# Optimization experiments

Measured on AMD Instinct MI355X. Metric: run time of the kernel, lower is better.

Reference implementation:

```python
import jax, jax.numpy as jnp
import numpy as np

EPS = 1e-8


def setup_inputs() -> dict:
    key = jax.random.key(0)
    ks = jax.random.split(key, 9)
    b, f, n1, n2 = 32, 256, 64, 256
    inp = {
        "search_feats": jax.random.normal(ks[0], (b, f, n2), jnp.float32),
        "template_feats": jax.random.normal(ks[1], (b, f, n1), jnp.float32),
        "template_seeds": jax.random.normal(ks[2], (b, n1, 3), jnp.float32),
        # SharedMLP (1x1 conv2d) weights: channels 260 -> 256 -> 256 -> 256
        "W1": jax.random.normal(ks[3], (256, 260), jnp.float32) * 0.05,
        "b1": jnp.zeros((256,), jnp.float32),
        "W2": jax.random.normal(ks[4], (256, 256), jnp.float32) * 0.05,
        "b2": jnp.zeros((256,), jnp.float32),
        "W3": jax.random.normal(ks[5], (256, 256), jnp.float32) * 0.05,
        "b3": jnp.zeros((256,), jnp.float32),
        # conv1d chain (kernel size 1): 256 -> 256 (ReLU) -> 256 (no act)
        "W4": jax.random.normal(ks[6], (256, 256), jnp.float32) * 0.05,
        "b4": jnp.zeros((256,), jnp.float32),
        "W5": jax.random.normal(ks[7], (256, 256), jnp.float32) * 0.05,
        "b5": jnp.zeros((256,), jnp.float32),
    }
    return inp


def reference(search_feats, template_feats, template_seeds,
              W1, b1, W2, b2, W3, b3, W4, b4, W5, b5):
    b, f, n2 = search_feats.shape
    n1 = template_feats.shape[-1]

    # Cosine similarity along feature dim (torch clamps each norm to eps).
    t_norm = template_feats / jnp.maximum(
        jnp.linalg.norm(template_feats, axis=1, keepdims=True), EPS)
    s_norm = search_feats / jnp.maximum(
        jnp.linalg.norm(search_feats, axis=1, keepdims=True), EPS)
    sim = jnp.einsum('bfn,bfm->bnm', t_norm, s_norm)  # (b, n1, n2)

    # Build fusion feature (b, 1+3+f, n1, n2) via broadcasting (no copies needed).
    xyz = jnp.transpose(template_seeds, (0, 2, 1))  # (b, 3, n1)
    xyz_b = jnp.broadcast_to(xyz[:, :, :, None], (b, 3, n1, n2))
    tf_b = jnp.broadcast_to(template_feats[:, :, :, None], (b, f, n1, n2))
    fusion = jnp.concatenate([sim[:, None], xyz_b, tf_b], axis=1)  # (b, 260, n1, n2)

    # SharedMLP: 1x1 conv2d + ReLU per layer
    x = jax.nn.relu(jnp.einsum('oc,bcnm->bonm', W1, fusion) + b1[None, :, None, None])
    x = jax.nn.relu(jnp.einsum('oc,bcnm->bonm', W2, x) + b2[None, :, None, None])
    x = jax.nn.relu(jnp.einsum('oc,bcnm->bonm', W3, x) + b3[None, :, None, None])

    # max_pool2d over n1 dim (kernel [n1, 1]) then squeeze -> (b, 256, n2)
    x = jnp.max(x, axis=2)

    # conv1d chain (kernel size 1)
    x = jax.nn.relu(jnp.einsum('oc,bcm->bom', W4, x) + b4[None, :, None])
    x = jnp.einsum('oc,bcm->bom', W5, x) + b5[None, :, None]
    return x
```

## Files before the change

kernel.cpp:

```cpp
#include <hip/hip_runtime.h>
#include <math.h>

#define BB 32
#define FF 256
#define N1 64
#define N2 256

typedef _Float16 f16;
typedef _Float16 f16x4 __attribute__((ext_vector_type(4)));
typedef _Float16 f16x8 __attribute__((ext_vector_type(8)));
typedef float f32x4 __attribute__((ext_vector_type(4)));

#define OFFB_W14T 0u
#define OFFB_W1H  45056u
#define OFFB_W2H  176128u
#define OFFB_W3H  307200u
#define OFFB_W4H  438272u
#define OFFB_W5H  569344u

__global__ void k_prep(const float* __restrict__ W1, const float* __restrict__ W2,
                       const float* __restrict__ W3, const float* __restrict__ W4,
                       const float* __restrict__ W5, char* __restrict__ wsb) {
  int x = blockIdx.x, m = blockIdx.y, t = threadIdx.x;
  int idx = x * 256 + t;
  if (m == 0)      ((f16*)(wsb + OFFB_W2H))[idx] = (f16)W2[idx];
  else if (m == 1) ((f16*)(wsb + OFFB_W3H))[idx] = (f16)W3[idx];
  else if (m == 2) ((f16*)(wsb + OFFB_W4H))[idx] = (f16)W4[idx];
  else if (m == 3) ((f16*)(wsb + OFFB_W5H))[idx] = (f16)W5[idx];
  else if (m == 4) ((f16*)(wsb + OFFB_W1H))[idx] = (f16)W1[x * 260 + 4 + t];
  else if (x < 4)  ((float*)(wsb + OFFB_W14T))[x * 256 + t] = W1[t * 260 + x];
}


#define LD(S, KS, MF) (*(const f16x8*)((S) + ((KS) * 2 + (MF)) * 1024 + lane * 16))

#define ZERO_ACC                                                  \
  _Pragma("unroll") for (int of = 0; of < 4; ++of)                \
  _Pragma("unroll") for (int mf = 0; mf < 2; ++mf)                \
      acc[of][mf] = (f32x4){0.f, 0.f, 0.f, 0.f};

#define GEMM4(SRC)                                                                \
  {                                                                               \
    f16x8 a0 = LD(SRC, 0, 0), a1 = LD(SRC, 0, 1);                                 \
    f16x8 p0 = LD(SRC, 1, 0), p1 = LD(SRC, 1, 1);                                 \
    __builtin_amdgcn_s_setprio(1);                                                \
    _Pragma("unroll") for (int ks = 0; ks < 8; ++ks) {                            \
      f16x8 c0 = a0, c1 = a1;                                                     \
      a0 = p0; a1 = p1;                                                           \
      if (ks < 6) { p0 = LD(SRC, ks + 2, 0); p1 = LD(SRC, ks + 2, 1); }           \
      _Pragma("unroll") for (int of = 0; of < 4; ++of) {                          \
        acc[of][0] = __builtin_amdgcn_mfma_f32_16x16x32_f16(wreg[of][ks], c0,     \
                                                            acc[of][0], 0, 0, 0); \
        acc[of][1] = __builtin_amdgcn_mfma_f32_16x16x32_f16(wreg[of][ks], c1,     \
                                                            acc[of][1], 0, 0, 0); \
      }                                                                           \
    }                                                                             \
    __builtin_amdgcn_s_setprio(0);                                                \
  }

#define STORE_FRAG(DST)                                                           \
  _Pragma("unroll") for (int of = 0; of < 4; ++of)                                \
  _Pragma("unroll") for (int mf = 0; mf < 2; ++mf) {                              \
    f16x4 hv;                                                                     \
    _Pragma("unroll") for (int j = 0; j < 4; ++j)                                 \
        hv[j] = (f16)fmaxf(acc[of][mf][j] + biasv[of][j], 0.f);                   \
    *(f16x4*)((DST) + ((wg * 2 + (of >> 1)) * 2 + mf) * 1024 +                    \
              ((of & 1) * 2 + (g >> 1)) * 256 + r * 16 + (g & 1) * 8) = hv;       \
  }

#define POOLUP                                                                    \
  _Pragma("unroll") for (int of = 0; of < 4; ++of)                                \
  _Pragma("unroll") for (int mf = 0; mf < 2; ++mf)                                \
  _Pragma("unroll") for (int j = 0; j < 4; ++j) {                                 \
    f16 hv = (f16)fmaxf(acc[of][mf][j] + biasv[of][j], 0.f);                      \
    if (hv > pool[of][mf][j]) pool[of][mf][j] = hv;                               \
  }

#define PRODUCE_Y1(NN, DST)                                                       \
  {                                                                               \
    float sv0 = sml[(NN) * 32 + r];                                               \
    float sv1 = sml[(NN) * 32 + 16 + r];                                          \
    f16x8 c8 = *(const f16x8*)(c1h + (NN) * 264 + w * 32 + g * 8);                \
    f16x8 h0, h1;                                                                 \
    _Pragma("unroll") for (int q = 0; q < 4; ++q) {                               \
      float ca = (float)c8[q], cb = (float)c8[4 + q];                             \
      h0[q] = (f16)fmaxf(fmaf(w1a[q], sv0, ca), 0.f);                             \
      h0[4 + q] = (f16)fmaxf(fmaf(w1b[q], sv0, cb), 0.f);                         \
      h1[q] = (f16)fmaxf(fmaf(w1a[q], sv1, ca), 0.f);                             \
      h1[4 + q] = (f16)fmaxf(fmaf(w1b[q], sv1, cb), 0.f);                         \
    }                                                                             \
    *(f16x8*)((DST) + (w * 2) * 1024 + lane * 16) = h0;                           \
    *(f16x8*)((DST) + (w * 2 + 1) * 1024 + lane * 16) = h1;                       \
  }

__global__ __launch_bounds__(512, 2) void k_mega(
    const float* __restrict__ sf, const float* __restrict__ tf,
    const float* __restrict__ seeds, const float* __restrict__ b1,
    const float* __restrict__ b2, const float* __restrict__ b3,
    const float* __restrict__ b4, const float* __restrict__ b5,
    const char* __restrict__ wsb, float* __restrict__ out) {
  const int mt = blockIdx.x, b = blockIdx.y, mb = mt * 32;
  const int tid = threadIdx.x;
  const int w = tid >> 6, lane = tid & 63, g = lane >> 4, r = lane & 15;
  const int grp = w >> 2, wg = w & 3;

  const float* w14t = (const float*)(wsb + OFFB_W14T);
  const f16* w1h = (const f16*)(wsb + OFFB_W1H);
  const f16* w2h = (const f16*)(wsb + OFFB_W2H);
  const f16* w3h = (const f16*)(wsb + OFFB_W3H);
  const f16* w4h = (const f16*)(wsb + OFFB_W4H);
  const f16* w5h = (const f16*)(wsb + OFFB_W5H);

  __shared__ __align__(16) char yl[65536];
  __shared__ __align__(16) f16 c1h[64 * 264];
  __shared__ __align__(16) float sml[64 * 32];
  __shared__ __align__(16) float part_t[64 * 8];
  __shared__ __align__(16) float part_s[32 * 16];
  __shared__ float invt_l[64];
  __shared__ float invs_l[32];
#define Y1BUF(i) (yl + (i) * 16384)
#define Y2BUF(i) (yl + 32768 + (i) * 16384)

  float tv[32];
  {
    const int n = lane;
    float ssq = 0.f;
#pragma unroll
    for (int j = 0; j < 4; ++j) {
      int oct = j * 8 + w;
#pragma unroll
      for (int e = 0; e < 8; ++e) {
        float v = tf[((size_t)b * FF + oct * 8 + e) * N1 + n];
        tv[j * 8 + e] = v;
        ssq = fmaf(v, v, ssq);
      }
    }
    part_t[n * 8 + w] = ssq;
  }
  float sv2[16];
  {
    const int m = tid & 31, q = tid >> 5;
    float ssq = 0.f;
#pragma unroll
    for (int j = 0; j < 2; ++j) {
      int oct = j * 16 + q;
#pragma unroll
      for (int e = 0; e < 8; ++e) {
        float v = sf[((size_t)b * FF + oct * 8 + e) * N2 + mb + m];
        sv2[j * 8 + e] = v;
        ssq = fmaf(v, v, ssq);
      }
    }
    part_s[m * 16 + q] = ssq;
  }
  __syncthreads();
  if (tid < 64) {
    float a = 0.f;
#pragma unroll
    for (int i = 0; i < 8; ++i) a += part_t[tid * 8 + i];
    invt_l[tid] = 1.0f / fmaxf(sqrtf(a), 1e-8f);
  }
  if (tid < 32) {
    float a = 0.f;
#pragma unroll
    for (int i = 0; i < 16; ++i) a += part_s[tid * 16 + i];
    invs_l[tid] = 1.0f / fmaxf(sqrtf(a), 1e-8f);
  }
  __syncthreads();
  {
    const int n = lane;
#pragma unroll
    for (int j = 0; j < 4; ++j) {
      int oct = j * 8 + w;
      f16x8 h;
#pragma unroll
      for (int e = 0; e < 8; ++e) h[e] = (f16)tv[j * 8 + e];
      *(f16x8*)(yl + ((oct >> 2) * 4 + (n >> 4)) * 1024 +
                ((oct & 3) * 16 + (n & 15)) * 16) = h;
    }
  }
  {
    const int m = tid & 31, q = tid >> 5;
    float iv = invs_l[m];
#pragma unroll
    for (int j = 0; j < 2; ++j) {
      int oct = j * 16 + q;
      f16x8 h;
#pragma unroll
      for (int e = 0; e < 8; ++e) h[e] = (f16)(sv2[j * 8 + e] * iv);
      *(f16x8*)(yl + 32768 + ((oct >> 2) * 2 + (m >> 4)) * 1024 +
                ((oct & 3) * 16 + (m & 15)) * 16) = h;
    }
  }
  __syncthreads();

  {
    const int nt = w >> 1, mfs = w & 1;
    f32x4 sa = {0.f, 0.f, 0.f, 0.f};
#pragma unroll
    for (int ks = 0; ks < 8; ++ks) {
      f16x8 af = *(const f16x8*)(yl + (ks * 4 + nt) * 1024 + lane * 16);
      f16x8 bfm = *(const f16x8*)(yl + 32768 + (ks * 2 + mfs) * 1024 + lane * 16);
      sa = __builtin_amdgcn_mfma_f32_16x16x32_f16(af, bfm, sa, 0, 0, 0);
    }
#pragma unroll
    for (int j = 0; j < 4; ++j) {
      int n = nt * 16 + g * 4 + j;
      sml[n * 32 + mfs * 16 + r] = sa[j] * invt_l[n];
    }
  }
  {
    f16x8 w1f[2][8];
#pragma unroll
    for (int ofl = 0; ofl < 2; ++ofl)
#pragma unroll
      for (int ks = 0; ks < 8; ++ks)
        w1f[ofl][ks] = *(const f16x8*)(w1h + (w * 32 + ofl * 16 + r) * 256 +
                                       ks * 32 + g * 8);
    f32x4 ac[2][4];
#pragma unroll
    for (int ofl = 0; ofl < 2; ++ofl)
#pragma unroll
      for (int nf = 0; nf < 4; ++nf) ac[ofl][nf] = (f32x4){0.f, 0.f, 0.f, 0.f};
#pragma unroll
    for (int ks = 0; ks < 8; ++ks)
#pragma unroll
      for (int nf = 0; nf < 4; ++nf) {
        f16x8 bfm = *(const f16x8*)(yl + (ks * 4 + nf) * 1024 + lane * 16);
        ac[0][nf] = __builtin_amdgcn_mfma_f32_16x16x32_f16(w1f[0][ks], bfm,
                                                           ac[0][nf], 0, 0, 0);
        ac[1][nf] = __builtin_amdgcn_mfma_f32_16x16x32_f16(w1f[1][ks], bfm,
                                                           ac[1][nf], 0, 0, 0);
      }
    f32x4 b1v[2], wx[2], wy[2], wz[2];
#pragma unroll
    for (int ofl = 0; ofl < 2; ++ofl) {
      int o = w * 32 + ofl * 16 + g * 4;
      b1v[ofl] = *(const f32x4*)(b1 + o);
      wx[ofl] = *(const f32x4*)(w14t + 256 + o);
      wy[ofl] = *(const f32x4*)(w14t + 512 + o);
      wz[ofl] = *(const f32x4*)(w14t + 768 + o);
    }
#pragma unroll
    for (int nf = 0; nf < 4; ++nf) {
      int n = nf * 16 + r;
      const float* sd = seeds + ((size_t)b * 64 + n) * 3;
      float sx = sd[0], sy = sd[1], sz = sd[2];
#pragma unroll
      for (int ofl = 0; ofl < 2; ++ofl) {
        f16x4 hv;
#pragma unroll
        for (int j = 0; j < 4; ++j)
          hv[j] = (f16)(ac[ofl][nf][j] + b1v[ofl][j] + wx[ofl][j] * sx +
                        wy[ofl][j] * sy + wz[ofl][j] * sz);
        *(f16x4*)(c1h + n * 264 + w * 32 + ofl * 16 + g * 4) = hv;
      }
    }
  }
  __syncthreads();

  f16x8 wreg[4][8];
  f32x4 biasv[4];
  f16x4 pool[4][2];
  f32x4 acc[4][2];
  f32x4 w1a, w1b;
  {
    const f16* wsrc = grp ? w3h : w2h;
    const float* bsrc = grp ? b3 : b2;
#pragma unroll
    for (int of = 0; of < 4; ++of) {
#pragma unroll
      for (int ks = 0; ks < 8; ++ks)
        wreg[of][ks] = *(const f16x8*)(wsrc + (wg * 64 + of * 16 + r) * 256 +
                                       ks * 32 + g * 8);
      biasv[of] = *(const f32x4*)(bsrc + wg * 64 + of * 16 + g * 4);
    }
    w1a = *(const f32x4*)(w14t + w * 32 + g * 8);
    w1b = *(const f32x4*)(w14t + w * 32 + g * 8 + 4);
  }
#pragma unroll
  for (int of = 0; of < 4; ++of)
#pragma unroll
    for (int mf = 0; mf < 2; ++mf) pool[of][mf] = (f16x4){0, 0, 0, 0};

  PRODUCE_Y1(0, Y1BUF(0));
  __syncthreads();

  for (int n = 0; n < N1; ++n) {
    if (grp == 0) {
      ZERO_ACC;
      GEMM4(Y1BUF(n & 1));
      if (n + 1 < N1) PRODUCE_Y1(n + 1, Y1BUF((n + 1) & 1));
      STORE_FRAG(Y2BUF(n & 1));
    } else {
      if (n + 1 < N1) PRODUCE_Y1(n + 1, Y1BUF((n + 1) & 1));
      if (n > 0) {
        ZERO_ACC;
        GEMM4(Y2BUF((n - 1) & 1));
        POOLUP;
      }
    }
    __syncthreads();
  }

  if (grp == 1) {
    ZERO_ACC;
    GEMM4(Y2BUF(1));
    POOLUP;
#pragma unroll
    for (int of = 0; of < 4; ++of)
#pragma unroll
      for (int mf = 0; mf < 2; ++mf)
        *(f16x4*)(Y1BUF(0) + ((wg * 2 + (of >> 1)) * 2 + mf) * 1024 +
                  ((of & 1) * 2 + (g >> 1)) * 256 + r * 16 + (g & 1) * 8) =
            pool[of][mf];
  } else {
#pragma unroll
    for (int of = 0; of < 4; ++of) {
#pragma unroll
      for (int ks = 0; ks < 8; ++ks)
        wreg[of][ks] = *(const f16x8*)(w4h + (wg * 64 + of * 16 + r) * 256 +
                                       ks * 32 + g * 8);
      biasv[of] = *(const f32x4*)(b4 + wg * 64 + of * 16 + g * 4);
    }
  }
  __syncthreads();
  if (grp == 0) {
    ZERO_ACC;
    GEMM4(Y1BUF(0));
    STORE_FRAG(Y2BUF(0));
  } else {
#pragma unroll
    for (int of = 0; of < 4; ++of) {
#pragma unroll
      for (int ks = 0; ks < 8; ++ks)
        wreg[of][ks] = *(const f16x8*)(w5h + (wg * 64 + of * 16 + r) * 256 +
                                       ks * 32 + g * 8);
      biasv[of] = *(const f32x4*)(b5 + wg * 64 + of * 16 + g * 4);
    }
  }
  __syncthreads();
  if (grp == 1) {
    ZERO_ACC;
    GEMM4(Y2BUF(0));
#pragma unroll
    for (int of = 0; of < 4; ++of)
#pragma unroll
      for (int mf = 0; mf < 2; ++mf) {
        float* op = out + ((size_t)(b * 256 + wg * 64 + of * 16 + g * 4)) * 256 +
                    mb + mf * 16 + r;
#pragma unroll
        for (int j = 0; j < 4; ++j)
          op[(size_t)j * 256] = acc[of][mf][j] + biasv[of][j];
      }
  }
}

extern "C" void kernel_launch(void* const* d_in, const int* in_sizes, int n_in,
                              void* d_out, int out_size, void* d_ws, size_t ws_size,
                              hipStream_t stream) {
  const float* sf = (const float*)d_in[0];
  const float* tf = (const float*)d_in[1];
  const float* seeds = (const float*)d_in[2];
  const float* W1 = (const float*)d_in[3];
  const float* b1 = (const float*)d_in[4];
  const float* W2 = (const float*)d_in[5];
  const float* b2 = (const float*)d_in[6];
  const float* W3 = (const float*)d_in[7];
  const float* b3 = (const float*)d_in[8];
  const float* W4 = (const float*)d_in[9];
  const float* b4 = (const float*)d_in[10];
  const float* W5 = (const float*)d_in[11];
  const float* b5 = (const float*)d_in[12];
  char* wsb = (char*)d_ws;
  float* out = (float*)d_out;

  k_prep<<<dim3(256, 6), 256, 0, stream>>>(W1, W2, W3, W4, W5, wsb);
  k_mega<<<dim3(8, BB), 512, 0, stream>>>(sf, tf, seeds, b1, b2, b3, b4, b5,
                                          wsb, out);
}
```

Measured before the change: 136.0 us.

## Process two n1 rows per barrier with 4-deep LDS ring, c1 in global

```diff
diff --git a/kernel.cpp b/kernel.cpp
--- a/kernel.cpp
+++ b/kernel.cpp
@@ -17,6 +17,7 @@
 #define OFFB_W3H  307200u
 #define OFFB_W4H  438272u
 #define OFFB_W5H  569344u
+#define OFFB_C1G  700416u
 
 __global__ void k_prep(const float* __restrict__ W1, const float* __restrict__ W2,
                        const float* __restrict__ W3, const float* __restrict__ W4,
@@ -32,22 +33,22 @@
 }
 
 
-#define LD(S, KS, MF) (*(const f16x8*)((S) + ((KS) * 2 + (MF)) * 1024 + lane * 16))
-
 #define ZERO_ACC                                                  \
   _Pragma("unroll") for (int of = 0; of < 4; ++of)                \
   _Pragma("unroll") for (int mf = 0; mf < 2; ++mf)                \
       acc[of][mf] = (f32x4){0.f, 0.f, 0.f, 0.f};
 
+#define LDF(S, KS, MF) (*(const f16x8*)((S) + ((KS) * 2 + (MF)) * 1024 + lane * 16))
+
 #define GEMM4(SRC)                                                                \
   {                                                                               \
-    f16x8 a0 = LD(SRC, 0, 0), a1 = LD(SRC, 0, 1);                                 \
-    f16x8 p0 = LD(SRC, 1, 0), p1 = LD(SRC, 1, 1);                                 \
+    f16x8 a0 = LDF(SRC, 0, 0), a1 = LDF(SRC, 0, 1);                               \
+    f16x8 p0 = LDF(SRC, 1, 0), p1 = LDF(SRC, 1, 1);                               \
     __builtin_amdgcn_s_setprio(1);                                                \
     _Pragma("unroll") for (int ks = 0; ks < 8; ++ks) {                            \
       f16x8 c0 = a0, c1 = a1;                                                     \
       a0 = p0; a1 = p1;                                                           \
-      if (ks < 6) { p0 = LD(SRC, ks + 2, 0); p1 = LD(SRC, ks + 2, 1); }           \
+      if (ks < 6) { p0 = LDF(SRC, ks + 2, 0); p1 = LDF(SRC, ks + 2, 1); }         \
       _Pragma("unroll") for (int of = 0; of < 4; ++of) {                          \
         acc[of][0] = __builtin_amdgcn_mfma_f32_16x16x32_f16(wreg[of][ks], c0,     \
                                                             acc[of][0], 0, 0, 0); \
@@ -76,21 +77,21 @@
     if (hv > pool[of][mf][j]) pool[of][mf][j] = hv;                               \
   }
 
-#define PRODUCE_Y1(NN, DST)                                                       \
+#define PRODUCE_ROW(NN, C8)                                                       \
   {                                                                               \
     float sv0 = sml[(NN) * 32 + r];                                               \
     float sv1 = sml[(NN) * 32 + 16 + r];                                          \
-    f16x8 c8 = *(const f16x8*)(c1h + (NN) * 264 + w * 32 + g * 8);                \
+    char* dst = Y1S(NN);                                                          \
     f16x8 h0, h1;                                                                 \
     _Pragma("unroll") for (int q = 0; q < 4; ++q) {                               \
-      float ca = (float)c8[q], cb = (float)c8[4 + q];                             \
+      float ca = (float)(C8)[q], cb = (float)(C8)[4 + q];                         \
       h0[q] = (f16)fmaxf(fmaf(w1a[q], sv0, ca), 0.f);                             \
       h0[4 + q] = (f16)fmaxf(fmaf(w1b[q], sv0, cb), 0.f);                         \
       h1[q] = (f16)fmaxf(fmaf(w1a[q], sv1, ca), 0.f);                             \
       h1[4 + q] = (f16)fmaxf(fmaf(w1b[q], sv1, cb), 0.f);                         \
     }                                                                             \
-    *(f16x8*)((DST) + (w * 2) * 1024 + lane * 16) = h0;                           \
-    *(f16x8*)((DST) + (w * 2 + 1) * 1024 + lane * 16) = h1;                       \
+    *(f16x8*)(dst + (w * 2) * 1024 + lane * 16) = h0;                             \
+    *(f16x8*)(dst + (w * 2 + 1) * 1024 + lane * 16) = h1;                         \
   }
 
 __global__ __launch_bounds__(512, 2) void k_mega(
@@ -98,7 +99,7 @@
     const float* __restrict__ seeds, const float* __restrict__ b1,
     const float* __restrict__ b2, const float* __restrict__ b3,
     const float* __restrict__ b4, const float* __restrict__ b5,
-    const char* __restrict__ wsb, float* __restrict__ out) {
+    char* __restrict__ wsb, float* __restrict__ out) {
   const int mt = blockIdx.x, b = blockIdx.y, mb = mt * 32;
   const int tid = threadIdx.x;
   const int w = tid >> 6, lane = tid & 63, g = lane >> 4, r = lane & 15;
@@ -110,16 +111,16 @@
   const f16* w3h = (const f16*)(wsb + OFFB_W3H);
   const f16* w4h = (const f16*)(wsb + OFFB_W4H);
   const f16* w5h = (const f16*)(wsb + OFFB_W5H);
-
-  __shared__ __align__(16) char yl[65536];
-  __shared__ __align__(16) f16 c1h[64 * 264];
-  __shared__ __align__(16) float sml[64 * 32];
-  __shared__ __align__(16) float part_t[64 * 8];
-  __shared__ __align__(16) float part_s[32 * 16];
-  __shared__ float invt_l[64];
-  __shared__ float invs_l[32];
-#define Y1BUF(i) (yl + (i) * 16384)
-#define Y2BUF(i) (yl + 32768 + (i) * 16384)
+  f16* c1b = (f16*)(wsb + OFFB_C1G) + (size_t)b * 16384;
+
+  __shared__ __align__(16) char arena[139648];
+#define Y1S(n) (arena + ((n) & 3) * 16384)
+#define Y2S(n) (arena + 65536 + ((n) & 3) * 16384)
+  float* sml = (float*)(arena + 131072);
+  float* invt_l = (float*)(arena + 139264);
+  float* invs_l = (float*)(arena + 139520);
+  float* part_t = (float*)(arena + 98304);
+  float* part_s = (float*)(arena + 98304 + 2048);
 
   float tv[32];
   {
@@ -175,7 +176,7 @@
       f16x8 h;
 #pragma unroll
       for (int e = 0; e < 8; ++e) h[e] = (f16)tv[j * 8 + e];
-      *(f16x8*)(yl + ((oct >> 2) * 4 + (n >> 4)) * 1024 +
+      *(f16x8*)(arena + ((oct >> 2) * 4 + (n >> 4)) * 1024 +
                 ((oct & 3) * 16 + (n & 15)) * 16) = h;
     }
   }
@@ -188,7 +189,7 @@
       f16x8 h;
 #pragma unroll
       for (int e = 0; e < 8; ++e) h[e] = (f16)(sv2[j * 8 + e] * iv);
-      *(f16x8*)(yl + 32768 + ((oct >> 2) * 2 + (m >> 4)) * 1024 +
+      *(f16x8*)(arena + 65536 + ((oct >> 2) * 2 + (m >> 4)) * 1024 +
                 ((oct & 3) * 16 + (m & 15)) * 16) = h;
     }
   }
@@ -199,8 +200,8 @@
     f32x4 sa = {0.f, 0.f, 0.f, 0.f};
 #pragma unroll
     for (int ks = 0; ks < 8; ++ks) {
-      f16x8 af = *(const f16x8*)(yl + (ks * 4 + nt) * 1024 + lane * 16);
-      f16x8 bfm = *(const f16x8*)(yl + 32768 + (ks * 2 + mfs) * 1024 + lane * 16);
+      f16x8 af = *(const f16x8*)(arena + (ks * 4 + nt) * 1024 + lane * 16);
+      f16x8 bfm = *(const f16x8*)(arena + 65536 + (ks * 2 + mfs) * 1024 + lane * 16);
       sa = __builtin_amdgcn_mfma_f32_16x16x32_f16(af, bfm, sa, 0, 0, 0);
     }
 #pragma unroll
@@ -226,7 +227,7 @@
     for (int ks = 0; ks < 8; ++ks)
 #pragma unroll
       for (int nf = 0; nf < 4; ++nf) {
-        f16x8 bfm = *(const f16x8*)(yl + (ks * 4 + nf) * 1024 + lane * 16);
+        f16x8 bfm = *(const f16x8*)(arena + (ks * 4 + nf) * 1024 + lane * 16);
         ac[0][nf] = __builtin_amdgcn_mfma_f32_16x16x32_f16(w1f[0][ks], bfm,
                                                            ac[0][nf], 0, 0, 0);
         ac[1][nf] = __builtin_amdgcn_mfma_f32_16x16x32_f16(w1f[1][ks], bfm,
@@ -253,7 +254,7 @@
         for (int j = 0; j < 4; ++j)
           hv[j] = (f16)(ac[ofl][nf][j] + b1v[ofl][j] + wx[ofl][j] * sx +
                         wy[ofl][j] * sy + wz[ofl][j] * sz);
-        *(f16x4*)(c1h + n * 264 + w * 32 + ofl * 16 + g * 4) = hv;
+        *(f16x4*)(c1b + n * 256 + w * 32 + ofl * 16 + g * 4) = hv;
       }
     }
   }
@@ -283,20 +284,37 @@
 #pragma unroll
     for (int mf = 0; mf < 2; ++mf) pool[of][mf] = (f16x4){0, 0, 0, 0};
 
-  PRODUCE_Y1(0, Y1BUF(0));
-  __syncthreads();
-
-  for (int n = 0; n < N1; ++n) {
+  {
+    f16x8 c80 = *(const f16x8*)(c1b + 0 * 256 + w * 32 + g * 8);
+    f16x8 c81 = *(const f16x8*)(c1b + 1 * 256 + w * 32 + g * 8);
+    PRODUCE_ROW(0, c80);
+    PRODUCE_ROW(1, c81);
+  }
+  __syncthreads();
+
+  for (int p = 0; p < 32; ++p) {
+    const int n0 = 2 * p;
+    f16x8 c8a, c8b;
+    if (p < 31) {
+      c8a = *(const f16x8*)(c1b + (n0 + 2) * 256 + w * 32 + g * 8);
+      c8b = *(const f16x8*)(c1b + (n0 + 3) * 256 + w * 32 + g * 8);
+    }
     if (grp == 0) {
       ZERO_ACC;
-      GEMM4(Y1BUF(n & 1));
-      if (n + 1 < N1) PRODUCE_Y1(n + 1, Y1BUF((n + 1) & 1));
-      STORE_FRAG(Y2BUF(n & 1));
+      GEMM4(Y1S(n0));
+      STORE_FRAG(Y2S(n0));
+      ZERO_ACC;
+      GEMM4(Y1S(n0 + 1));
+      STORE_FRAG(Y2S(n0 + 1));
+      if (p < 31) { PRODUCE_ROW(n0 + 2, c8a); PRODUCE_ROW(n0 + 3, c8b); }
     } else {
-      if (n + 1 < N1) PRODUCE_Y1(n + 1, Y1BUF((n + 1) & 1));
-      if (n > 0) {
+      if (p < 31) { PRODUCE_ROW(n0 + 2, c8a); PRODUCE_ROW(n0 + 3, c8b); }
+      if (p > 0) {
         ZERO_ACC;
-        GEMM4(Y2BUF((n - 1) & 1));
+        GEMM4(Y2S(n0 - 2));
+        POOLUP;
+        ZERO_ACC;
+        GEMM4(Y2S(n0 - 1));
         POOLUP;
       }
     }
@@ -305,13 +323,16 @@
 
   if (grp == 1) {
     ZERO_ACC;
-    GEMM4(Y2BUF(1));
+    GEMM4(Y2S(62));
     POOLUP;
+    ZERO_ACC;
+    GEMM4(Y2S(63));
+    POOLUP;
 #pragma unroll
     for (int of = 0; of < 4; ++of)
 #pragma unroll
       for (int mf = 0; mf < 2; ++mf)
-        *(f16x4*)(Y1BUF(0) + ((wg * 2 + (of >> 1)) * 2 + mf) * 1024 +
+        *(f16x4*)(Y1S(0) + ((wg * 2 + (of >> 1)) * 2 + mf) * 1024 +
                   ((of & 1) * 2 + (g >> 1)) * 256 + r * 16 + (g & 1) * 8) =
             pool[of][mf];
   } else {
@@ -327,8 +348,8 @@
   __syncthreads();
   if (grp == 0) {
     ZERO_ACC;
-    GEMM4(Y1BUF(0));
-    STORE_FRAG(Y2BUF(0));
+    GEMM4(Y1S(0));
+    STORE_FRAG(Y2S(0));
   } else {
 #pragma unroll
     for (int of = 0; of < 4; ++of) {
@@ -342,7 +363,7 @@
   __syncthreads();
   if (grp == 1) {
     ZERO_ACC;
-    GEMM4(Y2BUF(0));
+    GEMM4(Y2S(0));
 #pragma unroll
     for (int of = 0; of < 4; ++of)
 #pragma unroll
```

Measured after the change: 138.3 us. Within noise of the previous version (+1.7%).
